# Kernel tuning notes

Measured on AMD Instinct MI355X. Metric: run time of the kernel, lower is better.

The kernel has to match this reference:

```python
import jax, jax.numpy as jnp
import numpy as np

NH = 12
LEVEL = 4  # Lmin = 2**LEVEL = 16


def _build_sets(T, Lmin):
    l_list, r_list = [], []
    L = Lmin
    while L <= T:
        for i in range(T // L):
            l_list.append(i * L)
            r_list.append((i + 1) * L - 1)
        L *= 2
    return np.asarray(l_list, np.int32), np.asarray(r_list, np.int32)


def _get_slice(x_cum, l_idx, r_idx):
    # x_cum: [B,nh,T,hs]; returns inclusive range-sums x[l..r] via cumsum diffs
    r = x_cum[:, :, r_idx, :]
    l = x_cum[:, :, np.maximum(np.asarray(l_idx) - 1, 0), :]
    mask = (np.asarray(l_idx) >= 1).astype(x_cum.dtype)[None, None, :, None]
    return r - l * mask


def _get_slice_dyn(x_cum, l_idx, r_idx):
    # same but with traced/jnp indices (tail term)
    r = x_cum[:, :, r_idx, :]
    l = x_cum[:, :, jnp.maximum(l_idx - 1, 0), :]
    mask = (l_idx >= 1).astype(x_cum.dtype)[None, None, :, None]
    return r - l * mask


def setup_inputs() -> dict:
    key = jax.random.key(0)
    k0, k1, k2, k3 = jax.random.split(key, 4)
    B, T, C = 8, 2048, 768
    hs = C // NH
    s = 0.02
    return {
        "x": jax.random.normal(k0, (B, T, C), jnp.float32),
        "Wqkv": jax.random.normal(k1, (3 * C, C), jnp.float32) * s,
        "Wproj": jax.random.normal(k2, (C, C), jnp.float32) * s,
        "Wv": jax.random.normal(k3, (hs, hs * hs), jnp.float32) * s,
        "bv": jnp.zeros((hs,), jnp.float32),
    }


def reference(x, Wqkv, Wproj, Wv, bv):
    B, T, C = x.shape
    nh = NH
    hs = C // nh
    Lmin = 2 ** LEVEL
    scale = 1.0 / jnp.sqrt(jnp.asarray(hs, x.dtype))

    qkv = x @ Wqkv.T  # [B,T,3C]
    q, k, v0 = jnp.split(qkv, 3, axis=-1)
    q = q.reshape(B, T, nh, hs).transpose(0, 2, 1, 3)   # [B,nh,T,hs]
    k = k.reshape(B, T, nh, hs).transpose(0, 2, 1, 3)
    v0 = v0.reshape(B, T, nh, hs).transpose(0, 2, 1, 3)

    # v = v_proj(outer(k, v0).flatten)  == einsum with Wv reshaped [hs,hs,hs]
    Wv3 = Wv.reshape(hs, hs, hs)
    v = jnp.einsum('bhti,bhtj,eij->bhte', k, v0, Wv3) + bv

    k_cum = jnp.cumsum(k, axis=2)
    v_cum = jnp.cumsum(v, axis=2)

    l_idx, r_idx = _build_sets(T, Lmin)  # static dyadic sets
    K = _get_slice(k_cum, l_idx, r_idx)  # [B,nh,S,hs]
    V = _get_slice(v_cum, l_idx, r_idx)

    t_idx = jnp.arange(T)
    mask = t_idx[:, None] >= jnp.asarray(r_idx)[None, :]  # [T,S]
    logits = jnp.einsum('bhtd,bhsd->bhts', q, K) * scale
    logits = jnp.where(mask[None, None], logits, -jnp.inf)

    # tail: remainder within the current Lmin block
    l_tail = (t_idx // Lmin) * Lmin
    K_tail = _get_slice_dyn(k_cum, l_tail, t_idx)  # [B,nh,T,hs]
    V_tail = _get_slice_dyn(v_cum, l_tail, t_idx)
    tail_logits = jnp.sum(q * K_tail, axis=-1) * scale  # [B,nh,T]

    att = jax.nn.softmax(jnp.concatenate([logits, tail_logits[..., None]], axis=-1), axis=-1)
    out = jnp.einsum('bhts,bhsd->bhtd', att[..., :-1], V) + att[..., -1:] * V_tail
    out = out.transpose(0, 2, 1, 3).reshape(B, T, C)
    return out @ Wproj.T
```

## Files before the change

### kernel.cpp

```cpp
#include <hip/hip_runtime.h>


typedef float  f32x4  __attribute__((ext_vector_type(4)));
typedef _Float16 half8 __attribute__((ext_vector_type(8)));
typedef _Float16 half4 __attribute__((ext_vector_type(4)));

#define DEV __device__ __forceinline__
#define MFMA16(a, b, c) __builtin_amdgcn_mfma_f32_16x16x32_f16((a), (b), (c), 0, 0, 0)
#define GLOAD16(gp, lp)                                                  \
  __builtin_amdgcn_global_load_lds(                                      \
      (const __attribute__((address_space(1))) unsigned int*)(gp),       \
      (__attribute__((address_space(3))) unsigned int*)(lp), 16, 0, 0)

__global__ __launch_bounds__(256) void k_cast16(const float* __restrict__ in,
                                                _Float16* __restrict__ outh, int n4) {
  int i = blockIdx.x * 256 + threadIdx.x;
  if (i >= n4) return;
  f32x4 v = ((const f32x4*)in)[i];
  half4 o;
#pragma unroll
  for (int c = 0; c < 4; ++c) o[c] = (_Float16)v[c];
  ((half4*)outh)[i] = o;
}

__global__ __launch_bounds__(256, 3) void k_gemm_qkv(
    const _Float16* __restrict__ A16, const _Float16* __restrict__ B16,
    _Float16* __restrict__ qo, _Float16* __restrict__ ko, _Float16* __restrict__ v0o) {
  __shared__ _Float16 sA[128][64], sB[128][64];
  const int K = 768;
  int tid = threadIdx.x, lane = tid & 63, wave = tid >> 6;
  int l15 = lane & 15, g = lane >> 4;
  int wr = wave >> 1, wc = wave & 1;
  int wg = (blockIdx.x & 7) * 288 + (blockIdx.x >> 3);
  int n0 = (wg % 18) * 128, m0 = (wg / 18) * 128;
  f32x4 acc[4][4];
#pragma unroll
  for (int a = 0; a < 4; ++a)
#pragma unroll
    for (int b = 0; b < 4; ++b) acc[a][b] = f32x4{0.f, 0.f, 0.f, 0.f};
  int rsel = lane >> 3;
  int csel = (lane & 7) ^ rsel;
  for (int k0 = 0; k0 < K; k0 += 64) {
#pragma unroll
    for (int r = 0; r < 4; ++r) {
      int row = wave * 32 + r * 8 + rsel;
      GLOAD16(&A16[(size_t)(m0 + row) * K + k0 + csel * 8], &sA[wave * 32 + r * 8][0]);
      GLOAD16(&B16[(size_t)(n0 + row) * K + k0 + csel * 8], &sB[wave * 32 + r * 8][0]);
    }
    __syncthreads();
#pragma unroll
    for (int kk = 0; kk < 2; ++kk) {
      int kc = kk * 4 + g;
      int cc = ((kc ^ (l15 & 7)) << 3);
      half8 af[4], bf[4];
#pragma unroll
      for (int mf = 0; mf < 4; ++mf) af[mf] = *(const half8*)&sA[wr * 64 + mf * 16 + l15][cc];
#pragma unroll
      for (int nf = 0; nf < 4; ++nf) bf[nf] = *(const half8*)&sB[wc * 64 + nf * 16 + l15][cc];
#pragma unroll
      for (int mf = 0; mf < 4; ++mf)
#pragma unroll
        for (int nf = 0; nf < 4; ++nf)
          acc[mf][nf] = MFMA16(af[mf], bf[nf], acc[mf][nf]);
    }
    __syncthreads();
  }
  int sec = n0 / 768;
  int nb = n0 - sec * 768;
#pragma unroll
  for (int mf = 0; mf < 4; ++mf)
#pragma unroll
    for (int nf = 0; nf < 4; ++nf)
#pragma unroll
      for (int r = 0; r < 4; ++r) {
        int m = m0 + wr * 64 + mf * 16 + (g << 2) + r;
        int n = nb + wc * 64 + nf * 16 + l15;
        int b = m >> 11, t = m & 2047;
        int h = n >> 6, d = n & 63;
        size_t idx = (((size_t)b * 12 + h) * 2048 + t) * 64 + d;
        _Float16 val = (_Float16)acc[mf][nf][r];
        if (sec == 0) qo[idx] = val;
        else if (sec == 1) ko[idx] = val;
        else v0o[idx] = val;
      }
}

__global__ __launch_bounds__(256, 3) void k_veins(
    const _Float16* __restrict__ kh, const _Float16* __restrict__ v0g,
    const _Float16* __restrict__ Wvh, const float* __restrict__ bv,
    _Float16* __restrict__ vout) {
  __shared__ _Float16 ks[256][72];
  __shared__ _Float16 sB[2][64][64];
  int tid = threadIdx.x, lane = tid & 63, wave = tid >> 6;
  int l15 = lane & 15, g = lane >> 4, g8 = g << 3;
  size_t row0 = (size_t)blockIdx.x * 256;

  int srow_lo = wave * 8 + (lane >> 3);
  int scsrc = (lane & 7) ^ (lane >> 3);
  auto STAGE = [&](int b, int i) {
#pragma unroll
    for (int h = 0; h < 2; ++h) {
      GLOAD16(&Wvh[(size_t)(h * 32 + srow_lo) * 4096 + i * 64 + (scsrc << 3)],
              ((_Float16*)sB) + (size_t)b * 4096 + (h * 256 + wave * 64) * 8);
    }
  };

#pragma unroll
  for (int r = 0; r < 8; ++r) {
    int row = (tid >> 3) + r * 32;
    int c8 = (tid & 7) << 3;
    *(half8*)&ks[row][c8] = *(const half8*)&kh[(row0 + row) * 64 + c8];
  }
  half8 v0r[4][2];
#pragma unroll
  for (int mf = 0; mf < 4; ++mf) {
    size_t rb = (row0 + wave * 64 + mf * 16 + l15) * 64;
#pragma unroll
    for (int kk = 0; kk < 2; ++kk)
      v0r[mf][kk] = *(const half8*)&v0g[rb + kk * 32 + g8];
  }
  f32x4 acc[4][4];
#pragma unroll
  for (int a = 0; a < 4; ++a)
#pragma unroll
    for (int b = 0; b < 4; ++b) acc[a][b] = f32x4{0.f, 0.f, 0.f, 0.f};

  STAGE(0, 0);
  __syncthreads();
  int r0 = wave * 64 + l15;
  for (int i8 = 0; i8 < 8; ++i8) {
    half8 kr0 = *(const half8*)&ks[r0][i8 * 8];
    half8 kr1 = *(const half8*)&ks[r0 + 16][i8 * 8];
    half8 kr2 = *(const half8*)&ks[r0 + 32][i8 * 8];
    half8 kr3 = *(const half8*)&ks[r0 + 48][i8 * 8];
#pragma unroll
    for (int ii = 0; ii < 8; ++ii) {
      int i = i8 * 8 + ii;
      int cur = i & 1;
      if (i < 63) STAGE(cur ^ 1, i + 1);
      half8 b0[4], b1[4];
#pragma unroll
      for (int nf = 0; nf < 4; ++nf) {
        b0[nf] = *(const half8*)&sB[cur][nf * 16 + l15][((g ^ (l15 & 7)) << 3)];
        b1[nf] = *(const half8*)&sB[cur][nf * 16 + l15][(((4 + g) ^ (l15 & 7)) << 3)];
      }
      _Float16 kv0 = kr0[ii], kv1 = kr1[ii], kv2 = kr2[ii], kv3 = kr3[ii];
      {
        half8 a0 = v0r[0][0] * kv0, a1 = v0r[1][0] * kv1;
        half8 a2 = v0r[2][0] * kv2, a3 = v0r[3][0] * kv3;
#pragma unroll
        for (int nf = 0; nf < 4; ++nf) {
          acc[0][nf] = MFMA16(a0, b0[nf], acc[0][nf]);
          acc[1][nf] = MFMA16(a1, b0[nf], acc[1][nf]);
          acc[2][nf] = MFMA16(a2, b0[nf], acc[2][nf]);
          acc[3][nf] = MFMA16(a3, b0[nf], acc[3][nf]);
        }
      }
      {
        half8 a0 = v0r[0][1] * kv0, a1 = v0r[1][1] * kv1;
        half8 a2 = v0r[2][1] * kv2, a3 = v0r[3][1] * kv3;
#pragma unroll
        for (int nf = 0; nf < 4; ++nf) {
          acc[0][nf] = MFMA16(a0, b1[nf], acc[0][nf]);
          acc[1][nf] = MFMA16(a1, b1[nf], acc[1][nf]);
          acc[2][nf] = MFMA16(a2, b1[nf], acc[2][nf]);
          acc[3][nf] = MFMA16(a3, b1[nf], acc[3][nf]);
        }
      }
      __syncthreads();
    }
  }
#pragma unroll
  for (int mf = 0; mf < 4; ++mf)
#pragma unroll
    for (int nf = 0; nf < 4; ++nf) {
      int e = (nf << 4) + l15;
      float bve = bv[e];
#pragma unroll
      for (int r = 0; r < 4; ++r) {
        int row = wave * 64 + mf * 16 + (g << 2) + r;
        vout[(row0 + row) * 64 + e] = (_Float16)(acc[mf][nf][r] + bve);
      }
    }
}

__global__ __launch_bounds__(256) void k_segments(
    const _Float16* __restrict__ kmat, const _Float16* __restrict__ vmat,
    _Float16* __restrict__ Ks, _Float16* __restrict__ Vt) {
  __shared__ float Ls[255][64];
  int bh = blockIdx.x, tid = threadIdx.x;
  size_t bh2048 = (size_t)bh * 2048;
  for (int task = tid; task < 8192; task += 256) {
    int seg = task >> 6, d = task & 63;
    const _Float16* p = kmat + (bh2048 + seg * 16) * 64 + d;
    float s = 0.f;
#pragma unroll
    for (int u = 0; u < 16; ++u) s += (float)p[u * 64];
    Ls[seg][d] = s;
  }
  __syncthreads();
  {
    int bprev = 0, bcur = 128, cnt = 64;
    for (int lev = 1; lev < 8; ++lev) {
      for (int task = tid; task < cnt * 64; task += 256) {
        int i = task >> 6, d = task & 63;
        Ls[bcur + i][d] = Ls[bprev + 2 * i][d] + Ls[bprev + 2 * i + 1][d];
      }
      __syncthreads();
      bprev = bcur; bcur += cnt; cnt >>= 1;
    }
  }
  for (int task = tid; task < 16384; task += 256) {
    int seg = task >> 6;
    float v = (seg < 255) ? Ls[seg][task & 63] : 0.f;
    Ks[(size_t)bh * 16384 + task] = (_Float16)v;
  }
  __syncthreads();
  for (int task = tid; task < 8192; task += 256) {
    int seg = task >> 6, d = task & 63;
    const _Float16* p = vmat + (bh2048 + seg * 16) * 64 + d;
    float s = 0.f;
#pragma unroll
    for (int u = 0; u < 16; ++u) s += (float)p[u * 64];
    Ls[seg][d] = s;
  }
  __syncthreads();
  {
    int bprev = 0, bcur = 128, cnt = 64;
    for (int lev = 1; lev < 8; ++lev) {
      for (int task = tid; task < cnt * 64; task += 256) {
        int i = task >> 6, d = task & 63;
        Ls[bcur + i][d] = Ls[bprev + 2 * i][d] + Ls[bprev + 2 * i + 1][d];
      }
      __syncthreads();
      bprev = bcur; bcur += cnt; cnt >>= 1;
    }
  }
  for (int task = tid; task < 16384; task += 256) {
    int d = task >> 8, seg = task & 255;
    float v = (seg < 255) ? Ls[seg][d] : 0.f;
    Vt[(size_t)bh * 16384 + task] = (_Float16)v;
  }
}

__global__ __launch_bounds__(256, 2) void k_attn2(
    const _Float16* __restrict__ qm, const _Float16* __restrict__ km,
    const _Float16* __restrict__ vm,
    const _Float16* __restrict__ Ks, const _Float16* __restrict__ Vt,
    _Float16* __restrict__ outp) {
  __shared__ __align__(16) _Float16 P[4][16][280];
  __shared__ __align__(16) _Float16 tK[4][16][72];
  __shared__ __align__(16) _Float16 tV[4][16][72];
  int tid = threadIdx.x, lane = tid & 63, wave = tid >> 6;
  int orig = blockIdx.y * 32 + blockIdx.x;
  int wg = (orig & 7) * 384 + (orig >> 3);
  int tile = wg & 31, bh = wg >> 5;
  int t0 = tile * 64, tw0 = t0 + wave * 16;
  size_t bh2048 = (size_t)bh * 2048;
  int l15 = lane & 15, g = lane >> 4, g8 = g << 3;

  {
    const _Float16* kp = km + (bh2048 + tw0) * 64 + lane;
    const _Float16* vp = vm + (bh2048 + tw0) * 64 + lane;
    float ka = 0.f, va = 0.f;
#pragma unroll
    for (int t = 0; t < 16; ++t) {
      ka += (float)kp[t * 64];
      va += (float)vp[t * 64];
      tK[wave][t][lane] = (_Float16)ka;
      tV[wave][t][lane] = (_Float16)va;
    }
  }
  half8 qf[2];
  {
    const _Float16* qp = qm + (bh2048 + tw0 + l15) * 64 + g8;
    qf[0] = *(const half8*)qp;
    qf[1] = *(const half8*)(qp + 32);
  }
  unsigned mA = 0, mE = 0;
#pragma unroll
  for (int nf = 0; nf < 16; ++nf) {
    int seg = nf * 16 + l15;
    if (seg < 255) {
      int m = 256 - seg;
      int cl = 32 - __clz(m - 1);
      int lev = 8 - cl;
      int rdx = (seg - (256 - (256 >> lev)) + 1) * (16 << lev) - 1;
      if (rdx < tw0) mA |= 1u << nf;
      else if (rdx == tw0 + 15) mE |= 1u << nf;
    }
  }

  f32x4 acc[17];
#pragma unroll
  for (int i = 0; i < 17; ++i) acc[i] = f32x4{0.f, 0.f, 0.f, 0.f};
  const _Float16* KsB = Ks + (size_t)bh * 16384;
  half8 hf[4][4], hg[4][4];
#pragma unroll
  for (int ksl = 0; ksl < 4; ++ksl) {
    const _Float16* ph = KsB + (size_t)(ksl * 32 + l15) * 64 + g8;
    hf[ksl][0] = *(const half8*)ph;
    hf[ksl][1] = *(const half8*)(ph + 32);
    hf[ksl][2] = *(const half8*)(ph + 1024);
    hf[ksl][3] = *(const half8*)(ph + 1056);
  }
#pragma unroll
  for (int ksl = 0; ksl < 4; ++ksl) {
    const _Float16* ph = KsB + (size_t)((ksl + 4) * 32 + l15) * 64 + g8;
    hg[ksl][0] = *(const half8*)ph;
    hg[ksl][1] = *(const half8*)(ph + 32);
    hg[ksl][2] = *(const half8*)(ph + 1024);
    hg[ksl][3] = *(const half8*)(ph + 1056);
  }
  __builtin_amdgcn_s_setprio(1);
#pragma unroll
  for (int ksl = 0; ksl < 4; ++ksl) {
    acc[2 * ksl]     = MFMA16(qf[0], hf[ksl][0], acc[2 * ksl]);
    acc[2 * ksl]     = MFMA16(qf[1], hf[ksl][1], acc[2 * ksl]);
    acc[2 * ksl + 1] = MFMA16(qf[0], hf[ksl][2], acc[2 * ksl + 1]);
    acc[2 * ksl + 1] = MFMA16(qf[1], hf[ksl][3], acc[2 * ksl + 1]);
  }
#pragma unroll
  for (int ksl = 0; ksl < 4; ++ksl) {
    int nf = 2 * (ksl + 4);
    acc[nf]     = MFMA16(qf[0], hg[ksl][0], acc[nf]);
    acc[nf]     = MFMA16(qf[1], hg[ksl][1], acc[nf]);
    acc[nf + 1] = MFMA16(qf[0], hg[ksl][2], acc[nf + 1]);
    acc[nf + 1] = MFMA16(qf[1], hg[ksl][3], acc[nf + 1]);
  }
  {
    const _Float16* tp = &tK[wave][l15][g8];
    half8 t0f = *(const half8*)tp;
    half8 t1f = *(const half8*)(tp + 32);
    acc[16] = MFMA16(qf[0], t0f, acc[16]);
    acc[16] = MFMA16(qf[1], t1f, acc[16]);
  }
  __builtin_amdgcn_s_setprio(0);

  const _Float16* VB = Vt + (size_t)bh * 16384;
  half8 vta[4][4];
#pragma unroll
  for (int ksl = 0; ksl < 4; ++ksl)
#pragma unroll
    for (int n2 = 0; n2 < 4; ++n2)
      vta[ksl][n2] = *(const half8*)(VB + (size_t)(n2 * 16 + l15) * 256 + ksl * 32 + g8);

  const float c = 0.125f * 1.44269504f;
  float mx[4], sm[4], et[4];
#pragma unroll
  for (int r = 0; r < 4; ++r) {
    int tr = g * 4 + r;
    mx[r] = (l15 == tr) ? acc[16][r] * c : -3.0e38f;
  }
#pragma unroll
  for (int nf = 0; nf < 16; ++nf) {
    bool bA = (mA >> nf) & 1, bE = (mE >> nf) & 1;
#pragma unroll
    for (int r = 0; r < 4; ++r) {
      bool u = bA || (bE && g == 3 && r == 3);
      if (u) mx[r] = fmaxf(mx[r], acc[nf][r] * c);
    }
  }
#pragma unroll
  for (int off = 1; off < 16; off <<= 1)
#pragma unroll
    for (int r = 0; r < 4; ++r) mx[r] = fmaxf(mx[r], __shfl_xor(mx[r], off));
#pragma unroll
  for (int r = 0; r < 4; ++r) {
    int tr = g * 4 + r;
    et[r] = (l15 == tr) ? exp2f(acc[16][r] * c - mx[r]) : 0.f;
    sm[r] = et[r];
  }
#pragma unroll
  for (int nf = 0; nf < 16; ++nf) {
    bool bA = (mA >> nf) & 1, bE = (mE >> nf) & 1;
#pragma unroll
    for (int r = 0; r < 4; ++r) {
      bool u = bA || (bE && g == 3 && r == 3);
      float e = u ? exp2f(acc[nf][r] * c - mx[r]) : 0.f;
      acc[nf][r] = e;
      sm[r] += e;
    }
  }
#pragma unroll
  for (int off = 1; off < 16; off <<= 1)
#pragma unroll
    for (int r = 0; r < 4; ++r) sm[r] += __shfl_xor(sm[r], off);
  float inv[4];
#pragma unroll
  for (int r = 0; r < 4; ++r) inv[r] = 1.f / sm[r];

  {
    half4 z4 = {};
    *(half4*)&P[wave][lane >> 2][256 + (lane & 3) * 4] = z4;
  }
#pragma unroll
  for (int nf = 0; nf < 16; ++nf)
#pragma unroll
    for (int r = 0; r < 4; ++r)
      P[wave][g * 4 + r][nf * 16 + l15] = (_Float16)(acc[nf][r] * inv[r]);
#pragma unroll
  for (int r = 0; r < 4; ++r)
    if (l15 == g * 4 + r) P[wave][l15][256 + l15] = (_Float16)(et[r] * inv[r]);

  half8 vtb[4][4];
#pragma unroll
  for (int ksl = 0; ksl < 4; ++ksl)
#pragma unroll
    for (int n2 = 0; n2 < 4; ++n2)
      vtb[ksl][n2] = *(const half8*)(VB + (size_t)(n2 * 16 + l15) * 256 + (ksl + 4) * 32 + g8);
  f32x4 oa[4];
#pragma unroll
  for (int i = 0; i < 4; ++i) oa[i] = f32x4{0.f, 0.f, 0.f, 0.f};
  __builtin_amdgcn_s_setprio(1);
#pragma unroll
  for (int ksl = 0; ksl < 4; ++ksl) {
    half8 pa = *(const half8*)&P[wave][l15][ksl * 32 + g8];
#pragma unroll
    for (int n2 = 0; n2 < 4; ++n2)
      oa[n2] = MFMA16(pa, vta[ksl][n2], oa[n2]);
  }
#pragma unroll
  for (int ksl = 0; ksl < 4; ++ksl) {
    half8 pa = *(const half8*)&P[wave][l15][(ksl + 4) * 32 + g8];
#pragma unroll
    for (int n2 = 0; n2 < 4; ++n2)
      oa[n2] = MFMA16(pa, vtb[ksl][n2], oa[n2]);
  }
  {
    half8 pa = *(const half8*)&P[wave][l15][256 + (g & 1) * 8];
#pragma unroll
    for (int n2 = 0; n2 < 4; ++n2) {
      half8 vt = {};
      if (g < 2) {
#pragma unroll
        for (int jj = 0; jj < 8; ++jj) vt[jj] = tV[wave][g8 + jj][n2 * 16 + l15];
      }
      oa[n2] = MFMA16(pa, vt, oa[n2]);
    }
  }
  __builtin_amdgcn_s_setprio(0);
  int b = bh / 12, h = bh - b * 12;
  size_t obase = ((size_t)b * 2048 + tw0) * 768 + h * 64;
#pragma unroll
  for (int n2 = 0; n2 < 4; ++n2)
#pragma unroll
    for (int r = 0; r < 4; ++r)
      outp[obase + (size_t)(g * 4 + r) * 768 + n2 * 16 + l15] = (_Float16)oa[n2][r];
}

__global__ __launch_bounds__(256, 3) void k_gemm_proj(
    const _Float16* __restrict__ A16, const _Float16* __restrict__ B16,
    float* __restrict__ C) {
  __shared__ _Float16 sA[128][64], sB[128][64];
  const int K = 768;
  int tid = threadIdx.x, lane = tid & 63, wave = tid >> 6;
  int l15 = lane & 15, g = lane >> 4;
  int wr = wave >> 1, wc = wave & 1;
  int wg = (blockIdx.x & 7) * 96 + (blockIdx.x >> 3);
  int n0 = (wg % 6) * 128, m0 = (wg / 6) * 128;
  f32x4 acc[4][4];
#pragma unroll
  for (int a = 0; a < 4; ++a)
#pragma unroll
    for (int b = 0; b < 4; ++b) acc[a][b] = f32x4{0.f, 0.f, 0.f, 0.f};
  int rsel = lane >> 3;
  int csel = (lane & 7) ^ rsel;
  for (int k0 = 0; k0 < K; k0 += 64) {
#pragma unroll
    for (int r = 0; r < 4; ++r) {
      int row = wave * 32 + r * 8 + rsel;
      GLOAD16(&A16[(size_t)(m0 + row) * K + k0 + csel * 8], &sA[wave * 32 + r * 8][0]);
      GLOAD16(&B16[(size_t)(n0 + row) * K + k0 + csel * 8], &sB[wave * 32 + r * 8][0]);
    }
    __syncthreads();
#pragma unroll
    for (int kk = 0; kk < 2; ++kk) {
      int kc = kk * 4 + g;
      int cc = ((kc ^ (l15 & 7)) << 3);
      half8 af[4], bf[4];
#pragma unroll
      for (int mf = 0; mf < 4; ++mf) af[mf] = *(const half8*)&sA[wr * 64 + mf * 16 + l15][cc];
#pragma unroll
      for (int nf = 0; nf < 4; ++nf) bf[nf] = *(const half8*)&sB[wc * 64 + nf * 16 + l15][cc];
#pragma unroll
      for (int mf = 0; mf < 4; ++mf)
#pragma unroll
        for (int nf = 0; nf < 4; ++nf)
          acc[mf][nf] = MFMA16(af[mf], bf[nf], acc[mf][nf]);
    }
    __syncthreads();
  }
#pragma unroll
  for (int mf = 0; mf < 4; ++mf)
#pragma unroll
    for (int nf = 0; nf < 4; ++nf)
#pragma unroll
      for (int r = 0; r < 4; ++r) {
        int m = m0 + wr * 64 + mf * 16 + (g << 2) + r;
        int n = n0 + wc * 64 + nf * 16 + l15;
        C[(size_t)m * 768 + n] = acc[mf][nf][r];
      }
}

extern "C" void kernel_launch(void* const* d_in, const int* in_sizes, int n_in,
                              void* d_out, int out_size, void* d_ws, size_t ws_size,
                              hipStream_t stream) {
  const float* x = (const float*)d_in[0];
  const float* Wqkv = (const float*)d_in[1];
  const float* Wproj = (const float*)d_in[2];
  const float* Wv = (const float*)d_in[3];
  const float* bv = (const float*)d_in[4];
  float* out = (float*)d_out;
  char* ws = (char*)d_ws;
  size_t off = 0;
  auto alloc = [&](size_t bytes) -> void* {
    void* p = (void*)(ws + off);
    off += (bytes + 255) & ~(size_t)255;
    return p;
  };
  _Float16* x16  = (_Float16*)alloc(12582912ull * 2);
  _Float16* wq16 = (_Float16*)alloc(1769472ull * 2);
  _Float16* wv16 = (_Float16*)alloc(262144ull * 2 + 8192);
  _Float16* wp16 = (_Float16*)alloc(589824ull * 2);
  _Float16* q16  = (_Float16*)alloc(12582912ull * 2);
  _Float16* k16  = (_Float16*)alloc(12582912ull * 2);
  _Float16* v016 = (_Float16*)alloc(12582912ull * 2);
  _Float16* vm16 = (_Float16*)alloc(12582912ull * 2);
  _Float16* Ks   = (_Float16*)alloc(1572864ull * 2);
  _Float16* Vt   = (_Float16*)alloc(1572864ull * 2);
  _Float16* outp = (_Float16*)alloc(12582912ull * 2);

  k_cast16<<<dim3(12288), dim3(256), 0, stream>>>(x, x16, 3145728);
  k_cast16<<<dim3(1728), dim3(256), 0, stream>>>(Wqkv, wq16, 442368);
  k_cast16<<<dim3(256), dim3(256), 0, stream>>>(Wv, wv16, 65536);
  k_cast16<<<dim3(576), dim3(256), 0, stream>>>(Wproj, wp16, 147456);
  k_gemm_qkv<<<dim3(2304), dim3(256), 0, stream>>>(x16, wq16, q16, k16, v016);
  k_veins<<<dim3(768), dim3(256), 0, stream>>>(k16, v016, wv16, bv, vm16);
  k_segments<<<dim3(96), dim3(256), 0, stream>>>(k16, vm16, Ks, Vt);
  k_attn2<<<dim3(32, 96), dim3(256), 0, stream>>>(q16, k16, vm16, Ks, Vt, outp);
  k_gemm_proj<<<dim3(768), dim3(256), 0, stream>>>(outp, wp16, out);
}
```

Before: 345.5 us.

## Split tail prefix sums into separate kernel and defer softmax normalization

Moves the within-block cumulative sums of k and v out of the attention kernel into a new k_tails kernel that writes tail K and transposed tail V to global memory. The attention kernel now loads them directly, drops its tK/tV shared arrays and raises its occupancy hint from 2 to 4 blocks. Softmax normalization moves from scaling each P element to scaling the final output rows. The cost is an extra launch and about 50 MB of extra global writes and reads for the tail buffers.

```diff
diff --git a/kernel.cpp b/kernel.cpp
--- a/kernel.cpp
+++ b/kernel.cpp
@@ -243,34 +243,57 @@
   }
 }
 
-__global__ __launch_bounds__(256, 2) void k_attn2(
-    const _Float16* __restrict__ qm, const _Float16* __restrict__ km,
-    const _Float16* __restrict__ vm,
+__global__ __launch_bounds__(256) void k_tails(
+    const _Float16* __restrict__ km, const _Float16* __restrict__ vm,
+    _Float16* __restrict__ tKg, _Float16* __restrict__ tVt) {
+  int bh = blockIdx.x >> 3, seg16 = (blockIdx.x & 7) * 16;
+  int wave = threadIdx.x >> 6, lane = threadIdx.x & 63;
+  for (int task = wave; task < 32; task += 4) {
+    int blk = seg16 + (task >> 1);
+    size_t base = ((size_t)bh * 2048 + blk * 16) * 64 + lane;
+    if (!(task & 1)) {
+      float ka = 0.f;
+      _Float16* o = tKg + (((size_t)bh * 128 + blk) * 16) * 64 + lane;
+#pragma unroll
+      for (int t = 0; t < 16; ++t) {
+        ka += (float)km[base + t * 64];
+        o[t * 64] = (_Float16)ka;
+      }
+    } else {
+      float va = 0.f;
+      half8 lo = {}, hi = {};
+#pragma unroll
+      for (int t = 0; t < 8; ++t) {
+        va += (float)vm[base + t * 64];
+        lo[t] = (_Float16)va;
+      }
+#pragma unroll
+      for (int t = 0; t < 8; ++t) {
+        va += (float)vm[base + (t + 8) * 64];
+        hi[t] = (_Float16)va;
+      }
+      _Float16* o = tVt + (((size_t)bh * 128 + blk) * 64 + lane) * 16;
+      ((half8*)o)[0] = lo;
+      ((half8*)o)[1] = hi;
+    }
+  }
+}
+
+__global__ __launch_bounds__(256, 4) void k_attn2(
+    const _Float16* __restrict__ qm,
+    const _Float16* __restrict__ tKg, const _Float16* __restrict__ tVt,
     const _Float16* __restrict__ Ks, const _Float16* __restrict__ Vt,
     _Float16* __restrict__ outp) {
   __shared__ __align__(16) _Float16 P[4][16][280];
-  __shared__ __align__(16) _Float16 tK[4][16][72];
-  __shared__ __align__(16) _Float16 tV[4][16][72];
   int tid = threadIdx.x, lane = tid & 63, wave = tid >> 6;
   int orig = blockIdx.y * 32 + blockIdx.x;
   int wg = (orig & 7) * 384 + (orig >> 3);
   int tile = wg & 31, bh = wg >> 5;
   int t0 = tile * 64, tw0 = t0 + wave * 16;
+  int blkw = tile * 4 + wave;
   size_t bh2048 = (size_t)bh * 2048;
   int l15 = lane & 15, g = lane >> 4, g8 = g << 3;
 
-  {
-    const _Float16* kp = km + (bh2048 + tw0) * 64 + lane;
-    const _Float16* vp = vm + (bh2048 + tw0) * 64 + lane;
-    float ka = 0.f, va = 0.f;
-#pragma unroll
-    for (int t = 0; t < 16; ++t) {
-      ka += (float)kp[t * 64];
-      va += (float)vp[t * 64];
-      tK[wave][t][lane] = (_Float16)ka;
-      tV[wave][t][lane] = (_Float16)va;
-    }
-  }
   half8 qf[2];
   {
     const _Float16* qp = qm + (bh2048 + tw0 + l15) * 64 + g8;
@@ -295,7 +318,7 @@
 #pragma unroll
   for (int i = 0; i < 17; ++i) acc[i] = f32x4{0.f, 0.f, 0.f, 0.f};
   const _Float16* KsB = Ks + (size_t)bh * 16384;
-  half8 hf[4][4], hg[4][4];
+  half8 hf[4][4], hg[4][4], t0f, t1f;
 #pragma unroll
   for (int ksl = 0; ksl < 4; ++ksl) {
     const _Float16* ph = KsB + (size_t)(ksl * 32 + l15) * 64 + g8;
@@ -312,6 +335,11 @@
     hg[ksl][2] = *(const half8*)(ph + 1024);
     hg[ksl][3] = *(const half8*)(ph + 1056);
   }
+  {
+    const _Float16* tp = tKg + (((size_t)bh * 128 + blkw) * 16 + l15) * 64 + g8;
+    t0f = *(const half8*)tp;
+    t1f = *(const half8*)(tp + 32);
+  }
   __builtin_amdgcn_s_setprio(1);
 #pragma unroll
   for (int ksl = 0; ksl < 4; ++ksl) {
@@ -328,13 +356,8 @@
     acc[nf + 1] = MFMA16(qf[0], hg[ksl][2], acc[nf + 1]);
     acc[nf + 1] = MFMA16(qf[1], hg[ksl][3], acc[nf + 1]);
   }
-  {
-    const _Float16* tp = &tK[wave][l15][g8];
-    half8 t0f = *(const half8*)tp;
-    half8 t1f = *(const half8*)(tp + 32);
-    acc[16] = MFMA16(qf[0], t0f, acc[16]);
-    acc[16] = MFMA16(qf[1], t1f, acc[16]);
-  }
+  acc[16] = MFMA16(qf[0], t0f, acc[16]);
+  acc[16] = MFMA16(qf[1], t1f, acc[16]);
   __builtin_amdgcn_s_setprio(0);
 
   const _Float16* VB = Vt + (size_t)bh * 16384;
@@ -398,10 +421,10 @@
   for (int nf = 0; nf < 16; ++nf)
 #pragma unroll
     for (int r = 0; r < 4; ++r)
-      P[wave][g * 4 + r][nf * 16 + l15] = (_Float16)(acc[nf][r] * inv[r]);
+      P[wave][g * 4 + r][nf * 16 + l15] = (_Float16)acc[nf][r];
 #pragma unroll
   for (int r = 0; r < 4; ++r)
-    if (l15 == g * 4 + r) P[wave][l15][256 + l15] = (_Float16)(et[r] * inv[r]);
+    if (l15 == g * 4 + r) P[wave][l15][256 + l15] = (_Float16)et[r];
 
   half8 vtb[4][4];
 #pragma unroll
@@ -429,13 +452,12 @@
   }
   {
     half8 pa = *(const half8*)&P[wave][l15][256 + (g & 1) * 8];
+    const _Float16* tvb = tVt + ((size_t)bh * 128 + blkw) * 1024;
 #pragma unroll
     for (int n2 = 0; n2 < 4; ++n2) {
       half8 vt = {};
-      if (g < 2) {
-#pragma unroll
-        for (int jj = 0; jj < 8; ++jj) vt[jj] = tV[wave][g8 + jj][n2 * 16 + l15];
-      }
+      if (g < 2)
+        vt = *(const half8*)(tvb + (size_t)(n2 * 16 + l15) * 16 + g8);
       oa[n2] = MFMA16(pa, vt, oa[n2]);
     }
   }
@@ -446,7 +468,7 @@
   for (int n2 = 0; n2 < 4; ++n2)
 #pragma unroll
     for (int r = 0; r < 4; ++r)
-      outp[obase + (size_t)(g * 4 + r) * 768 + n2 * 16 + l15] = (_Float16)oa[n2][r];
+      outp[obase + (size_t)(g * 4 + r) * 768 + n2 * 16 + l15] = (_Float16)(oa[n2][r] * inv[r]);
 }
 
 __global__ __launch_bounds__(256, 3) void k_gemm_proj(
@@ -529,6 +551,8 @@
   _Float16* vm16 = (_Float16*)alloc(12582912ull * 2);
   _Float16* Ks   = (_Float16*)alloc(1572864ull * 2);
   _Float16* Vt   = (_Float16*)alloc(1572864ull * 2);
+  _Float16* tKg  = (_Float16*)alloc(12582912ull * 2);
+  _Float16* tVt  = (_Float16*)alloc(12582912ull * 2);
   _Float16* outp = (_Float16*)alloc(12582912ull * 2);
 
   k_cast16<<<dim3(12288), dim3(256), 0, stream>>>(x, x16, 3145728);
@@ -538,6 +562,7 @@
   k_gemm_qkv<<<dim3(2304), dim3(256), 0, stream>>>(x16, wq16, q16, k16, v016);
   k_veins<<<dim3(768), dim3(256), 0, stream>>>(k16, v016, wv16, bv, vm16);
   k_segments<<<dim3(96), dim3(256), 0, stream>>>(k16, vm16, Ks, Vt);
-  k_attn2<<<dim3(32, 96), dim3(256), 0, stream>>>(q16, k16, vm16, Ks, Vt, outp);
+  k_tails<<<dim3(768), dim3(256), 0, stream>>>(k16, vm16, tKg, tVt);
+  k_attn2<<<dim3(32, 96), dim3(256), 0, stream>>>(q16, tKg, tVt, Ks, Vt, outp);
   k_gemm_proj<<<dim3(768), dim3(256), 0, stream>>>(outp, wp16, out);
 }
```

Result: slower. 443.8 us (+28.5%).
